# Kernel tuning notes

Measured on AMD Instinct MI355X. Metric: run time of the kernel, lower is better.

## Reference

```python
import jax, jax.numpy as jnp
import numpy as np

TAU = 2.0      # spikingjelly LIF default membrane time constant
VTH = 1.0      # threshold
SCALE = 0.25
NUM_HEADS = 16
EPS = 1e-5


def lif(x):
    # single-step LIF from rest (v=0, v_reset=0): u = v + (x - v)/tau = x/tau; spike = H(u - vth)
    return (x / TAU >= VTH).astype(x.dtype)


def bn(z, gamma, beta, mean, var):
    # inference-mode BatchNorm1d over channel dim of (TB, C, N)
    inv = gamma / jnp.sqrt(var + EPS)
    return z * inv[:, None] + (beta - mean * inv)[:, None]


def branch(z, w, gamma, beta, mean, var):
    # conv1x1 (pointwise channel mix) -> BN -> LIF
    z = jnp.einsum('oc,bcn->bon', w, z)
    return lif(bn(z, gamma, beta, mean, var))


def setup_inputs() -> dict:
    key = jax.random.key(0)
    ks = jax.random.split(key, 8)
    T, B, C, N = 4, 2, 512, 512
    x = jax.random.normal(ks[0], (T, B, C, N), dtype=jnp.float32)
    y = jax.random.normal(ks[1], (T, B, C, N), dtype=jnp.float32)
    def conv_w(k):
        return jax.random.normal(k, (C, C), dtype=jnp.float32) / np.float32(np.sqrt(C))
    def bn_params(k):
        km, kv = jax.random.split(k)
        gamma = jnp.full((C,), 2.0, dtype=jnp.float32)  # scale so LIF spikes are non-trivially sparse
        beta = jnp.zeros((C,), dtype=jnp.float32)
        mean = 0.1 * jax.random.normal(km, (C,), dtype=jnp.float32)
        var = 0.5 + jax.random.uniform(kv, (C,), dtype=jnp.float32)
        return gamma, beta, mean, var
    q_g, q_b, q_m, q_v = bn_params(ks[2])
    k_g, k_b, k_m, k_v = bn_params(ks[3])
    v_g, v_b, v_m, v_v = bn_params(ks[4])
    p_g, p_b, p_m, p_v = bn_params(ks[5])
    return {
        'x': x, 'y': y,
        'q_w': conv_w(jax.random.fold_in(key, 10)), 'q_g': q_g, 'q_b': q_b, 'q_m': q_m, 'q_v': q_v,
        'k_w': conv_w(jax.random.fold_in(key, 11)), 'k_g': k_g, 'k_b': k_b, 'k_m': k_m, 'k_v': k_v,
        'v_w': conv_w(jax.random.fold_in(key, 12)), 'v_g': v_g, 'v_b': v_b, 'v_m': v_m, 'v_v': v_v,
        'p_w': conv_w(jax.random.fold_in(key, 13)), 'p_g': p_g, 'p_b': p_b, 'p_m': p_m, 'p_v': p_v,
    }


def reference(x, y, q_w, q_g, q_b, q_m, q_v, k_w, k_g, k_b, k_m, k_v,
              v_w, v_g, v_b, v_m, v_v, p_w, p_g, p_b, p_m, p_v):
    T, B, C, N = x.shape
    H = NUM_HEADS
    D = C // H
    xq = x.reshape(T * B, C, N)
    yk = y.reshape(T * B, C, N)
    # q/k/v: conv1x1 + BN + LIF, then split heads: (T,B,C,N) -> (T,B,H,N,D)
    q = branch(xq, q_w, q_g, q_b, q_m, q_v).reshape(T, B, H, D, N).transpose(0, 1, 2, 4, 3)
    k = branch(yk, k_w, k_g, k_b, k_m, k_v).reshape(T, B, H, D, N).transpose(0, 1, 2, 4, 3)
    v = branch(yk, v_w, v_g, v_b, v_m, v_v).reshape(T, B, H, D, N).transpose(0, 1, 2, 4, 3)
    # softmax-free spiking attention: (Q K^T) V * scale
    attn = jnp.einsum('tbhnd,tbhmd->tbhnm', q, k)
    o = jnp.einsum('tbhnm,tbhmd->tbhnd', attn, v) * SCALE
    o = o.transpose(0, 1, 2, 4, 3).reshape(T, B, C, N)  # (T,B,H,D,N) -> (T,B,C,N)
    o = lif(o.reshape(T * B, C, N))
    o = branch(o, p_w, p_g, p_b, p_m, p_v).reshape(T, B, C, N)
    return o
```

## Files before the change

kernel.cpp:

```cpp
#include <hip/hip_runtime.h>
#include <math.h>

#define TBD 8
#define CD  512
#define ND  512
#define PLANE (TBD*CD*ND)
#define WPL   (CD*CD)

typedef __attribute__((ext_vector_type(8))) short bf16x8;
typedef __attribute__((ext_vector_type(4))) float f32x4;

__device__ __forceinline__ float b2f(unsigned short u){
  union{unsigned int i; float f;} x; x.i = ((unsigned int)u) << 16; return x.f;
}
__device__ __forceinline__ unsigned short f2b(float f){
  unsigned int u = __builtin_bit_cast(unsigned int, f);
  u += 0x7fffu + ((u >> 16) & 1u);
  return (unsigned short)(u >> 16);
}
__device__ __forceinline__ void async_ld16(const unsigned short* g, unsigned short* l){
  __builtin_amdgcn_global_load_lds((const __attribute__((address_space(1))) unsigned int*)g,
      (__attribute__((address_space(3))) unsigned int*)l, 16, 0, 0);
}

__global__ __launch_bounds__(256) void prep(
    const float* __restrict__ x, const float* __restrict__ y,
    const float* __restrict__ Qw, const float* __restrict__ Kw,
    const float* __restrict__ Vw, const float* __restrict__ Pw,
    const float* __restrict__ Qg, const float* __restrict__ Qb, const float* __restrict__ Qm, const float* __restrict__ Qv,
    const float* __restrict__ Kg, const float* __restrict__ Kb, const float* __restrict__ Km, const float* __restrict__ Kv,
    const float* __restrict__ Vg, const float* __restrict__ Vb, const float* __restrict__ Vm, const float* __restrict__ Vv,
    const float* __restrict__ Pg, const float* __restrict__ Pb, const float* __restrict__ Pm, const float* __restrict__ Pv,
    unsigned short* __restrict__ wsu, float* __restrict__ ib)
{
  const int bx = blockIdx.x, t = threadIdx.x;
  if (bx < 1024) {
    __shared__ __align__(16) float tl[64][68];
    const int inp = bx >> 9, rem = bx & 511;
    const int tb = rem >> 6, tile = rem & 63;
    const int ct = (tile & 7) << 6, nt = (tile >> 3) << 6;
    const float* xg = inp ? y : x;
    #pragma unroll
    for (int r = 0; r < 4; ++r) {
      const int row = (t >> 4) + (r << 4);
      const int col = (t & 15) << 2;
      *(float4*)&tl[row][col] =
          *(const float4*)(xg + ((size_t)(tb*CD + ct + row))*ND + nt + col);
    }
    __syncthreads();
    const int nl = t >> 2, cb = (t & 3) << 4;
    __align__(16) unsigned short h[3][16];
    #pragma unroll
    for (int j = 0; j < 16; ++j) {
      const float f = tl[cb + j][nl];
      const unsigned short a = f2b(f);  const float r1 = f - b2f(a);
      const unsigned short b = f2b(r1); const float r2 = r1 - b2f(b);
      h[0][j] = a; h[1][j] = b; h[2][j] = f2b(r2);
    }
    unsigned short* base = wsu + (size_t)inp*3*PLANE;
    const size_t rowo = ((size_t)tb*ND + nt + nl)*CD + ct + cb;
    #pragma unroll
    for (int s = 0; s < 3; ++s) {
      *(uint4*)(base + (size_t)s*PLANE + rowo)     = *(uint4*)&h[s][0];
      *(uint4*)(base + (size_t)s*PLANE + rowo + 8) = *(uint4*)&h[s][8];
    }
  } else if (bx < 2048) {
    const int b2 = bx - 1024;
    const int mat = b2 >> 8, rr = b2 & 255;
    const float* Wg = (mat==0)?Qw:(mat==1)?Kw:(mat==2)?Vw:Pw;
    const int row = (rr << 1) + (t >> 7);
    const int col = (t & 127) << 2;
    const float4 w = *(const float4*)(Wg + (size_t)row*CD + col);
    const float f[4] = {w.x, w.y, w.z, w.w};
    __align__(8) unsigned short h[3][4];
    #pragma unroll
    for (int j = 0; j < 4; ++j) {
      const unsigned short a = f2b(f[j]);  const float r1 = f[j] - b2f(a);
      const unsigned short b = f2b(r1);    const float r2 = r1 - b2f(b);
      h[0][j] = a; h[1][j] = b; h[2][j] = f2b(r2);
    }
    unsigned short* base = wsu + (size_t)6*PLANE + (size_t)mat*3*WPL;
    #pragma unroll
    for (int s = 0; s < 3; ++s)
      *(uint2*)(base + (size_t)s*WPL + (size_t)row*CD + col) = *(uint2*)&h[s][0];
  } else {
    const int idx = (bx - 2048)*256 + t;
    const int br = idx >> 9, ch = idx & 511;
    const float* G = (br==0)?Qg:(br==1)?Kg:(br==2)?Vg:Pg;
    const float* B = (br==0)?Qb:(br==1)?Kb:(br==2)?Vb:Pb;
    const float* M = (br==0)?Qm:(br==1)?Km:(br==2)?Vm:Pm;
    const float* V = (br==0)?Qv:(br==1)?Kv:(br==2)?Vv:Pv;
    const float inv = G[ch] / sqrtf(V[ch] + 1e-5f);
    ib[br*1024 + ch]       = inv;
    ib[br*1024 + 512 + ch] = B[ch] - M[ch]*inv;
  }
}

template<int XS, bool F32OUT>
__global__ __launch_bounds__(256) void gemm_mfma(
    const unsigned short* __restrict__ Ab,
    const unsigned short* __restrict__ Bbp,
    const float* __restrict__ ibp,
    unsigned short* __restrict__ outb,
    float* __restrict__ outf)
{
  const int bx  = blockIdx.x;
  const int idx = bx & 511;
  const int br  = bx >> 9;
  const int tb  = idx & 7;
  const int o0  = ((idx >> 3) & 7) << 6;
  const int n0  = (idx >> 6) << 6;
  const int t    = threadIdx.x;
  const int lane = t & 63, wave = t >> 6;

  const unsigned short* A = Ab + (size_t)br*3*WPL;
  const unsigned short* B = Bbp + (size_t)(br ? 3 : 0)*PLANE;
  const float* IB = ibp + br*1024;

  __shared__ __align__(16) unsigned short Al[2][3][4][512];
  __shared__ __align__(16) unsigned short Bl[2][XS][4][512];

  const int lr = lane >> 2;
  const int lc = (((lane & 3) ^ ((lane >> 3) & 3)) << 3);
  constexpr int TPW = (12 + 4*XS) / 4;

  auto stage = [&](int buf, int c0) {
    #pragma unroll
    for (int j = 0; j < TPW; ++j) {
      const int tix = wave*TPW + j;
      if (tix < 12) {
        const int s = tix >> 2, ot = tix & 3;
        const unsigned short* g = A + (size_t)s*WPL
            + (size_t)(o0 + (ot << 4) + lr)*CD + c0 + lc;
        async_ld16(g, &Al[buf][s][ot][lane << 3]);
      } else {
        const int k = tix - 12, s = k >> 2, nt = k & 3;
        const unsigned short* g = B + (size_t)s*PLANE
            + ((size_t)tb*ND + n0 + (nt << 4) + lr)*CD + c0 + lc;
        async_ld16(g, &Bl[buf][s][nt][lane << 3]);
      }
    }
  };

  f32x4 acc[2][2];
  const f32x4 zero = {0.f, 0.f, 0.f, 0.f};
  acc[0][0] = zero; acc[0][1] = zero; acc[1][0] = zero; acc[1][1] = zero;

  const int otb = (wave >> 1) << 1;
  const int ntb = (wave & 1) << 1;
  const int fo = ((lane & 15) << 5) + ((((lane >> 4) ^ ((lane >> 1) & 3)) & 3) << 3);

  stage(0, 0);
  for (int i = 0; i < 16; ++i) {
    const int buf = i & 1;
    __syncthreads();
    if (i < 15) stage(buf ^ 1, (i + 1) << 5);

    bf16x8 Af[3][2], Bf[XS][2];
    #pragma unroll
    for (int s = 0; s < 3; ++s)
      #pragma unroll
      for (int oy = 0; oy < 2; ++oy)
        Af[s][oy] = *(const bf16x8*)&Al[buf][s][otb + oy][fo];
    #pragma unroll
    for (int s = 0; s < XS; ++s)
      #pragma unroll
      for (int nx = 0; nx < 2; ++nx)
        Bf[s][nx] = *(const bf16x8*)&Bl[buf][s][ntb + nx][fo];

    auto mm = [&](int sa, int sb) {
      #pragma unroll
      for (int oy = 0; oy < 2; ++oy)
        #pragma unroll
        for (int nx = 0; nx < 2; ++nx)
          acc[oy][nx] = __builtin_amdgcn_mfma_f32_16x16x32_bf16(
              Af[sa][oy], Bf[sb][nx], acc[oy][nx], 0, 0, 0);
    };
    if constexpr (XS == 3) {
      mm(0,0); mm(0,1); mm(1,0); mm(1,1); mm(0,2); mm(2,0);
    } else {
      mm(0,0); mm(1,0); mm(2,0);
    }
  }

  const int rbase = (lane >> 4) << 2;
  const int cl = lane & 15;
  #pragma unroll
  for (int oy = 0; oy < 2; ++oy) {
    #pragma unroll
    for (int r = 0; r < 4; ++r) {
      const int ch = o0 + ((otb + oy) << 4) + rbase + r;
      const float inv  = IB[ch];
      const float bias = IB[512 + ch];
      #pragma unroll
      for (int nx = 0; nx < 2; ++nx) {
        const float v = acc[oy][nx][r];
        const bool sp = (v * inv + bias >= 2.0f);
        const int n = n0 + ((ntb + nx) << 4) + cl;
        const size_t off = ((size_t)tb*CD + ch)*ND + n;
        if constexpr (F32OUT) outf[off] = sp ? 1.0f : 0.0f;
        else (outb + (size_t)br*PLANE)[off] = sp ? (unsigned short)0x3F80 : (unsigned short)0;
      }
    }
  }
}

__global__ __launch_bounds__(256) void attn(
    const unsigned short* __restrict__ Qs, const unsigned short* __restrict__ Ks,
    const unsigned short* __restrict__ Vs, unsigned short* __restrict__ S2T)
{
  const int tbh = blockIdx.x >> 2;
  const int n0  = (blockIdx.x & 3) << 7;
  const int t   = threadIdx.x;

  __shared__ __align__(16) float sm[2*32*260];
  float* Ksh = sm;
  float* Vsh = sm + 32*260;
  float* Gs  = sm;
  float* Osh = sm + 2048;

  const unsigned short* Kh = Ks + (size_t)tbh*32*ND;
  const unsigned short* Vh = Vs + (size_t)tbh*32*ND;
  const unsigned short* Qh = Qs + (size_t)tbh*32*ND;

  const int d1a = t >> 4, d2a = t & 15;
  float a00 = 0.f, a01 = 0.f, a10 = 0.f, a11 = 0.f;
  const int srow = t & 31, scb = (t >> 5) << 5;

  for (int m0 = 0; m0 < ND; m0 += 256) {
    if (m0) __syncthreads();
    #pragma unroll
    for (int q = 0; q < 4; ++q) {
      const uint4 kraw = *(const uint4*)(Kh + (size_t)srow*ND + m0 + scb + (q<<3));
      const uint4 vraw = *(const uint4*)(Vh + (size_t)srow*ND + m0 + scb + (q<<3));
      const unsigned short* kr = (const unsigned short*)&kraw;
      const unsigned short* vr = (const unsigned short*)&vraw;
      float4 k0 = {b2f(kr[0]), b2f(kr[1]), b2f(kr[2]), b2f(kr[3])};
      float4 k1 = {b2f(kr[4]), b2f(kr[5]), b2f(kr[6]), b2f(kr[7])};
      float4 v0 = {b2f(vr[0]), b2f(vr[1]), b2f(vr[2]), b2f(vr[3])};
      float4 v1 = {b2f(vr[4]), b2f(vr[5]), b2f(vr[6]), b2f(vr[7])};
      *(float4*)&Ksh[srow*260 + scb + (q<<3)]     = k0;
      *(float4*)&Ksh[srow*260 + scb + (q<<3) + 4] = k1;
      *(float4*)&Vsh[srow*260 + scb + (q<<3)]     = v0;
      *(float4*)&Vsh[srow*260 + scb + (q<<3) + 4] = v1;
    }
    __syncthreads();
    #pragma unroll 8
    for (int m = 0; m < 256; m += 4) {
      const float4 k0 = *(const float4*)&Ksh[d1a*260 + m];
      const float4 k1 = *(const float4*)&Ksh[(d1a+16)*260 + m];
      const float4 v0 = *(const float4*)&Vsh[d2a*260 + m];
      const float4 v1 = *(const float4*)&Vsh[(d2a+16)*260 + m];
      a00 += k0.x*v0.x + k0.y*v0.y + k0.z*v0.z + k0.w*v0.w;
      a01 += k0.x*v1.x + k0.y*v1.y + k0.z*v1.z + k0.w*v1.w;
      a10 += k1.x*v0.x + k1.y*v0.y + k1.z*v0.z + k1.w*v0.w;
      a11 += k1.x*v1.x + k1.y*v1.y + k1.z*v1.z + k1.w*v1.w;
    }
  }
  __syncthreads();
  Gs[d1a*33 + d2a]           = a00;
  Gs[d1a*33 + d2a + 16]      = a01;
  Gs[(d1a+16)*33 + d2a]      = a10;
  Gs[(d1a+16)*33 + d2a + 16] = a11;
  __syncthreads();

  const int r  = t >> 5;
  const int nn = (t & 31) << 2;
  float o[4][4];
  #pragma unroll
  for (int j = 0; j < 4; ++j)
    #pragma unroll
    for (int u = 0; u < 4; ++u) o[j][u] = 0.f;

  #pragma unroll 4
  for (int dp = 0; dp < 32; ++dp) {
    const uint2 qraw = *(const uint2*)(Qh + (size_t)dp*ND + n0 + nn);
    const unsigned short* qr = (const unsigned short*)&qraw;
    const float q0 = b2f(qr[0]), q1 = b2f(qr[1]), q2 = b2f(qr[2]), q3 = b2f(qr[3]);
    #pragma unroll
    for (int j = 0; j < 4; ++j) {
      const float gv = Gs[dp*33 + r + (j<<3)];
      o[j][0] += q0*gv; o[j][1] += q1*gv; o[j][2] += q2*gv; o[j][3] += q3*gv;
    }
  }
  #pragma unroll
  for (int j = 0; j < 4; ++j)
    #pragma unroll
    for (int u = 0; u < 4; ++u)
      Osh[(nn+u)*36 + r + (j<<3)] = o[j][u];
  __syncthreads();

  const int n   = t >> 1;
  const int cb2 = (t & 1) << 4;
  __align__(16) unsigned short h[16];
  #pragma unroll
  for (int j = 0; j < 16; j += 4) {
    const float4 f = *(const float4*)&Osh[n*36 + cb2 + j];
    h[j]   = (f.x >= 8.0f) ? 0x3F80 : 0;
    h[j+1] = (f.y >= 8.0f) ? 0x3F80 : 0;
    h[j+2] = (f.z >= 8.0f) ? 0x3F80 : 0;
    h[j+3] = (f.w >= 8.0f) ? 0x3F80 : 0;
  }
  const int tb = tbh >> 4, hh = tbh & 15;
  unsigned short* dst = S2T + ((size_t)tb*ND + n0 + n)*CD + (hh << 5) + cb2;
  *(uint4*)(dst)     = *(uint4*)&h[0];
  *(uint4*)(dst + 8) = *(uint4*)&h[8];
}

extern "C" void kernel_launch(void* const* d_in, const int* in_sizes, int n_in,
                              void* d_out, int out_size, void* d_ws, size_t ws_size,
                              hipStream_t stream)
{
  const float* x  = (const float*)d_in[0];
  const float* y  = (const float*)d_in[1];
  const float* qw = (const float*)d_in[2];
  const float* qg = (const float*)d_in[3];
  const float* qb = (const float*)d_in[4];
  const float* qm = (const float*)d_in[5];
  const float* qv = (const float*)d_in[6];
  const float* kw = (const float*)d_in[7];
  const float* kg = (const float*)d_in[8];
  const float* kb = (const float*)d_in[9];
  const float* km = (const float*)d_in[10];
  const float* kv = (const float*)d_in[11];
  const float* vw = (const float*)d_in[12];
  const float* vg = (const float*)d_in[13];
  const float* vb = (const float*)d_in[14];
  const float* vm = (const float*)d_in[15];
  const float* vv = (const float*)d_in[16];
  const float* pw = (const float*)d_in[17];
  const float* pg = (const float*)d_in[18];
  const float* pb = (const float*)d_in[19];
  const float* pm = (const float*)d_in[20];
  const float* pv = (const float*)d_in[21];

  unsigned short* wsu = (unsigned short*)d_ws;
  unsigned short* Wq  = wsu + (size_t)6*PLANE;
  unsigned short* SPK = wsu + (size_t)6*PLANE + 12*WPL;
  unsigned short* S2T = SPK + (size_t)3*PLANE;
  float* ib = (float*)(wsu + (size_t)10*PLANE + 12*WPL);

  prep<<<2056, 256, 0, stream>>>(x, y, qw, kw, vw, pw,
      qg, qb, qm, qv, kg, kb, km, kv, vg, vb, vm, vv, pg, pb, pm, pv,
      wsu, ib);

  gemm_mfma<3, false><<<1536, 256, 0, stream>>>(Wq, wsu, ib, SPK, nullptr);

  attn<<<512, 256, 0, stream>>>(SPK, SPK + PLANE, SPK + 2*(size_t)PLANE, S2T);

  gemm_mfma<1, true><<<512, 256, 0, stream>>>(Wq + (size_t)9*WPL, S2T,
      ib + 3*1024, nullptr, (float*)d_out);
}
```

Measured before the change: 186.8 us.

## Move spiking attention onto fp16 MFMA with transposed Q and staged epilogues

The attention kernel's scalar fp32 K·V^T and G·Q loops are replaced by fp16 MFMA. K and V are loaded asynchronously into LDS and the Gram matrix is converted to fp16 per wave before multiplying by Q. The first GEMM now writes spikes as fp16 ones, and the Q branch is written transposed (n-major) so attention can read it directly. Both GEMM epilogues stage their output through LDS to produce coalesced vector stores. G entries are integer counts up to 512, which fp16 represents exactly. The risk is extra LDS traffic and added synchronisation in the epilogues.

After: 175.5 us. 6.0% less time.

```diff
diff --git a/kernel.cpp b/kernel.cpp
--- a/kernel.cpp
+++ b/kernel.cpp
@@ -7,20 +7,24 @@
 #define PLANE (TBD*CD*ND)
 #define WPL   (CD*CD)
 
+typedef unsigned short u16;
+typedef unsigned int u32;
+typedef _Float16 f16;
 typedef __attribute__((ext_vector_type(8))) short bf16x8;
+typedef __attribute__((ext_vector_type(8))) _Float16 f16x8;
 typedef __attribute__((ext_vector_type(4))) float f32x4;
 
-__device__ __forceinline__ float b2f(unsigned short u){
-  union{unsigned int i; float f;} x; x.i = ((unsigned int)u) << 16; return x.f;
-}
-__device__ __forceinline__ unsigned short f2b(float f){
-  unsigned int u = __builtin_bit_cast(unsigned int, f);
+__device__ __forceinline__ float b2f(u16 u){
+  union{u32 i; float f;} x; x.i = ((u32)u) << 16; return x.f;
+}
+__device__ __forceinline__ u16 f2b(float f){
+  u32 u = __builtin_bit_cast(u32, f);
   u += 0x7fffu + ((u >> 16) & 1u);
-  return (unsigned short)(u >> 16);
-}
-__device__ __forceinline__ void async_ld16(const unsigned short* g, unsigned short* l){
-  __builtin_amdgcn_global_load_lds((const __attribute__((address_space(1))) unsigned int*)g,
-      (__attribute__((address_space(3))) unsigned int*)l, 16, 0, 0);
+  return (u16)(u >> 16);
+}
+__device__ __forceinline__ void async_ld16(const void* g, void* l){
+  __builtin_amdgcn_global_load_lds((const __attribute__((address_space(1))) u32*)g,
+      (__attribute__((address_space(3))) u32*)l, 16, 0, 0);
 }
 
 __global__ __launch_bounds__(256) void prep(
@@ -31,7 +35,7 @@
     const float* __restrict__ Kg, const float* __restrict__ Kb, const float* __restrict__ Km, const float* __restrict__ Kv,
     const float* __restrict__ Vg, const float* __restrict__ Vb, const float* __restrict__ Vm, const float* __restrict__ Vv,
     const float* __restrict__ Pg, const float* __restrict__ Pb, const float* __restrict__ Pm, const float* __restrict__ Pv,
-    unsigned short* __restrict__ wsu, float* __restrict__ ib)
+    u16* __restrict__ wsu, float* __restrict__ ib)
 {
   const int bx = blockIdx.x, t = threadIdx.x;
   if (bx < 1024) {
@@ -49,15 +53,15 @@
     }
     __syncthreads();
     const int nl = t >> 2, cb = (t & 3) << 4;
-    __align__(16) unsigned short h[3][16];
+    __align__(16) u16 h[3][16];
     #pragma unroll
     for (int j = 0; j < 16; ++j) {
       const float f = tl[cb + j][nl];
-      const unsigned short a = f2b(f);  const float r1 = f - b2f(a);
-      const unsigned short b = f2b(r1); const float r2 = r1 - b2f(b);
+      const u16 a = f2b(f);  const float r1 = f - b2f(a);
+      const u16 b = f2b(r1); const float r2 = r1 - b2f(b);
       h[0][j] = a; h[1][j] = b; h[2][j] = f2b(r2);
     }
-    unsigned short* base = wsu + (size_t)inp*3*PLANE;
+    u16* base = wsu + (size_t)inp*3*PLANE;
     const size_t rowo = ((size_t)tb*ND + nt + nl)*CD + ct + cb;
     #pragma unroll
     for (int s = 0; s < 3; ++s) {
@@ -72,14 +76,14 @@
     const int col = (t & 127) << 2;
     const float4 w = *(const float4*)(Wg + (size_t)row*CD + col);
     const float f[4] = {w.x, w.y, w.z, w.w};
-    __align__(8) unsigned short h[3][4];
+    __align__(8) u16 h[3][4];
     #pragma unroll
     for (int j = 0; j < 4; ++j) {
-      const unsigned short a = f2b(f[j]);  const float r1 = f[j] - b2f(a);
-      const unsigned short b = f2b(r1);    const float r2 = r1 - b2f(b);
+      const u16 a = f2b(f[j]);  const float r1 = f[j] - b2f(a);
+      const u16 b = f2b(r1);    const float r2 = r1 - b2f(b);
       h[0][j] = a; h[1][j] = b; h[2][j] = f2b(r2);
     }
-    unsigned short* base = wsu + (size_t)6*PLANE + (size_t)mat*3*WPL;
+    u16* base = wsu + (size_t)6*PLANE + (size_t)mat*3*WPL;
     #pragma unroll
     for (int s = 0; s < 3; ++s)
       *(uint2*)(base + (size_t)s*WPL + (size_t)row*CD + col) = *(uint2*)&h[s][0];
@@ -96,13 +100,11 @@
   }
 }
 
-template<int XS, bool F32OUT>
+template<int XS>
 __global__ __launch_bounds__(256) void gemm_mfma(
-    const unsigned short* __restrict__ Ab,
-    const unsigned short* __restrict__ Bbp,
+    const u16* __restrict__ Ab, const u16* __restrict__ Bbp,
     const float* __restrict__ ibp,
-    unsigned short* __restrict__ outb,
-    float* __restrict__ outf)
+    u16* __restrict__ qt, u16* __restrict__ spk, float* __restrict__ outf)
 {
   const int bx  = blockIdx.x;
   const int idx = bx & 511;
@@ -113,15 +115,16 @@
   const int t    = threadIdx.x;
   const int lane = t & 63, wave = t >> 6;
 
-  const unsigned short* A = Ab + (size_t)br*3*WPL;
-  const unsigned short* B = Bbp + (size_t)(br ? 3 : 0)*PLANE;
+  const u16* A = Ab + (size_t)br*3*WPL;
+  const u16* B = Bbp + (size_t)(br ? 3 : 0)*PLANE;
   const float* IB = ibp + br*1024;
 
-  __shared__ __align__(16) unsigned short Al[2][3][4][512];
-  __shared__ __align__(16) unsigned short Bl[2][XS][4][512];
+  __shared__ __align__(16) u16 smem[2*3*4*512 + 2*XS*4*512];
+  u16* Al = smem;
+  u16* Bl = smem + 2*3*4*512;
 
   const int lr = lane >> 2;
-  const int lc = (((lane & 3) ^ ((lane >> 3) & 3)) << 3);
+  const int lc = ((lane & 3) ^ ((lane >> 3) & 3)) << 3;
   constexpr int TPW = (12 + 4*XS) / 4;
 
   auto stage = [&](int buf, int c0) {
@@ -130,14 +133,12 @@
       const int tix = wave*TPW + j;
       if (tix < 12) {
         const int s = tix >> 2, ot = tix & 3;
-        const unsigned short* g = A + (size_t)s*WPL
-            + (size_t)(o0 + (ot << 4) + lr)*CD + c0 + lc;
-        async_ld16(g, &Al[buf][s][ot][lane << 3]);
+        async_ld16(A + (size_t)s*WPL + (size_t)(o0 + (ot<<4) + lr)*CD + c0 + lc,
+                   Al + (((buf*3 + s)*4 + ot) << 9) + (lane << 3));
       } else {
         const int k = tix - 12, s = k >> 2, nt = k & 3;
-        const unsigned short* g = B + (size_t)s*PLANE
-            + ((size_t)tb*ND + n0 + (nt << 4) + lr)*CD + c0 + lc;
-        async_ld16(g, &Bl[buf][s][nt][lane << 3]);
+        async_ld16(B + (size_t)s*PLANE + ((size_t)tb*ND + n0 + (nt<<4) + lr)*CD + c0 + lc,
+                   Bl + (((buf*XS + s)*4 + nt) << 9) + (lane << 3));
       }
     }
   };
@@ -161,12 +162,12 @@
     for (int s = 0; s < 3; ++s)
       #pragma unroll
       for (int oy = 0; oy < 2; ++oy)
-        Af[s][oy] = *(const bf16x8*)&Al[buf][s][otb + oy][fo];
+        Af[s][oy] = *(const bf16x8*)(Al + (((buf*3 + s)*4 + otb + oy) << 9) + fo);
     #pragma unroll
     for (int s = 0; s < XS; ++s)
       #pragma unroll
       for (int nx = 0; nx < 2; ++nx)
-        Bf[s][nx] = *(const bf16x8*)&Bl[buf][s][ntb + nx][fo];
+        Bf[s][nx] = *(const bf16x8*)(Bl + (((buf*XS + s)*4 + ntb + nx) << 9) + fo);
 
     auto mm = [&](int sa, int sb) {
       #pragma unroll
@@ -183,128 +184,168 @@
     }
   }
 
+  __syncthreads();
   const int rbase = (lane >> 4) << 2;
   const int cl = lane & 15;
-  #pragma unroll
-  for (int oy = 0; oy < 2; ++oy) {
-    #pragma unroll
-    for (int r = 0; r < 4; ++r) {
-      const int ch = o0 + ((otb + oy) << 4) + rbase + r;
-      const float inv  = IB[ch];
-      const float bias = IB[512 + ch];
-      #pragma unroll
-      for (int nx = 0; nx < 2; ++nx) {
-        const float v = acc[oy][nx][r];
-        const bool sp = (v * inv + bias >= 2.0f);
-        const int n = n0 + ((ntb + nx) << 4) + cl;
-        const size_t off = ((size_t)tb*CD + ch)*ND + n;
-        if constexpr (F32OUT) outf[off] = sp ? 1.0f : 0.0f;
-        else (outb + (size_t)br*PLANE)[off] = sp ? (unsigned short)0x3F80 : (unsigned short)0;
-      }
+
+  if constexpr (XS == 1) {
+    float* Fb = (float*)smem;
+    #pragma unroll
+    for (int oy = 0; oy < 2; ++oy)
+      #pragma unroll
+      for (int r = 0; r < 4; ++r) {
+        const int chl = ((otb + oy) << 4) + rbase + r;
+        const int ch = o0 + chl;
+        const float inv = IB[ch], bias = IB[512 + ch];
+        #pragma unroll
+        for (int nx = 0; nx < 2; ++nx) {
+          const bool sp = (acc[oy][nx][r] * inv + bias >= 2.0f);
+          Fb[chl*68 + ((ntb + nx) << 4) + cl] = sp ? 1.0f : 0.0f;
+        }
+      }
+    __syncthreads();
+    const int row = t >> 2, seg = (t & 3) << 4;
+    float* dst = outf + ((size_t)tb*CD + o0 + row)*ND + n0 + seg;
+    #pragma unroll
+    for (int u = 0; u < 4; ++u)
+      *(float4*)(dst + 4*u) = *(float4*)&Fb[row*68 + seg + 4*u];
+  } else {
+    u16* Sb = smem;
+    #pragma unroll
+    for (int oy = 0; oy < 2; ++oy)
+      #pragma unroll
+      for (int r = 0; r < 4; ++r) {
+        const int chl = ((otb + oy) << 4) + rbase + r;
+        const int ch = o0 + chl;
+        const float inv = IB[ch], bias = IB[512 + ch];
+        #pragma unroll
+        for (int nx = 0; nx < 2; ++nx) {
+          const bool sp = (acc[oy][nx][r] * inv + bias >= 2.0f);
+          Sb[chl*136 + ((ntb + nx) << 4) + cl] = sp ? (u16)0x3C00 : (u16)0;
+        }
+      }
+    __syncthreads();
+    if (br == 0) {
+      const int nr = t >> 2, cs = (t & 3) << 4;
+      __align__(16) u16 h[16];
+      #pragma unroll
+      for (int j = 0; j < 16; ++j) h[j] = Sb[(cs + j)*136 + nr];
+      u16* dst = qt + ((size_t)tb*ND + n0 + nr)*CD + o0 + cs;
+      *(uint4*)dst       = *(uint4*)&h[0];
+      *(uint4*)(dst + 8) = *(uint4*)&h[8];
+    } else {
+      u16* sp_ = spk + (size_t)(br - 1)*PLANE;
+      const int row = t >> 2, seg = (t & 3) << 4;
+      u16* dst = sp_ + ((size_t)tb*CD + o0 + row)*ND + n0 + seg;
+      *(uint4*)dst       = *(uint4*)&Sb[row*136 + seg];
+      *(uint4*)(dst + 8) = *(uint4*)&Sb[row*136 + seg + 8];
     }
   }
 }
 
 __global__ __launch_bounds__(256) void attn(
-    const unsigned short* __restrict__ Qs, const unsigned short* __restrict__ Ks,
-    const unsigned short* __restrict__ Vs, unsigned short* __restrict__ S2T)
+    const u16* __restrict__ Qt, const u16* __restrict__ Ks,
+    const u16* __restrict__ Vs, u16* __restrict__ S2T)
 {
   const int tbh = blockIdx.x >> 2;
   const int n0  = (blockIdx.x & 3) << 7;
-  const int t   = threadIdx.x;
-
-  __shared__ __align__(16) float sm[2*32*260];
-  float* Ksh = sm;
-  float* Vsh = sm + 32*260;
-  float* Gs  = sm;
-  float* Osh = sm + 2048;
-
-  const unsigned short* Kh = Ks + (size_t)tbh*32*ND;
-  const unsigned short* Vh = Vs + (size_t)tbh*32*ND;
-  const unsigned short* Qh = Qs + (size_t)tbh*32*ND;
-
-  const int d1a = t >> 4, d2a = t & 15;
-  float a00 = 0.f, a01 = 0.f, a10 = 0.f, a11 = 0.f;
-  const int srow = t & 31, scb = (t >> 5) << 5;
-
-  for (int m0 = 0; m0 < ND; m0 += 256) {
-    if (m0) __syncthreads();
-    #pragma unroll
-    for (int q = 0; q < 4; ++q) {
-      const uint4 kraw = *(const uint4*)(Kh + (size_t)srow*ND + m0 + scb + (q<<3));
-      const uint4 vraw = *(const uint4*)(Vh + (size_t)srow*ND + m0 + scb + (q<<3));
-      const unsigned short* kr = (const unsigned short*)&kraw;
-      const unsigned short* vr = (const unsigned short*)&vraw;
-      float4 k0 = {b2f(kr[0]), b2f(kr[1]), b2f(kr[2]), b2f(kr[3])};
-      float4 k1 = {b2f(kr[4]), b2f(kr[5]), b2f(kr[6]), b2f(kr[7])};
-      float4 v0 = {b2f(vr[0]), b2f(vr[1]), b2f(vr[2]), b2f(vr[3])};
-      float4 v1 = {b2f(vr[4]), b2f(vr[5]), b2f(vr[6]), b2f(vr[7])};
-      *(float4*)&Ksh[srow*260 + scb + (q<<3)]     = k0;
-      *(float4*)&Ksh[srow*260 + scb + (q<<3) + 4] = k1;
-      *(float4*)&Vsh[srow*260 + scb + (q<<3)]     = v0;
-      *(float4*)&Vsh[srow*260 + scb + (q<<3) + 4] = v1;
-    }
-    __syncthreads();
-    #pragma unroll 8
-    for (int m = 0; m < 256; m += 4) {
-      const float4 k0 = *(const float4*)&Ksh[d1a*260 + m];
-      const float4 k1 = *(const float4*)&Ksh[(d1a+16)*260 + m];
-      const float4 v0 = *(const float4*)&Vsh[d2a*260 + m];
-      const float4 v1 = *(const float4*)&Vsh[(d2a+16)*260 + m];
-      a00 += k0.x*v0.x + k0.y*v0.y + k0.z*v0.z + k0.w*v0.w;
-      a01 += k0.x*v1.x + k0.y*v1.y + k0.z*v1.z + k0.w*v1.w;
-      a10 += k1.x*v0.x + k1.y*v0.y + k1.z*v0.z + k1.w*v0.w;
-      a11 += k1.x*v1.x + k1.y*v1.y + k1.z*v1.z + k1.w*v1.w;
-    }
-  }
-  __syncthreads();
-  Gs[d1a*33 + d2a]           = a00;
-  Gs[d1a*33 + d2a + 16]      = a01;
-  Gs[(d1a+16)*33 + d2a]      = a10;
-  Gs[(d1a+16)*33 + d2a + 16] = a11;
-  __syncthreads();
-
-  const int r  = t >> 5;
-  const int nn = (t & 31) << 2;
-  float o[4][4];
+  const int t = threadIdx.x, lane = t & 63, wave = t >> 6;
+  const int tb = tbh >> 4, h = tbh & 15;
+
+  __shared__ __align__(16) u16 Kt[2*8*512];
+  __shared__ __align__(16) u16 Vt[2*8*512];
+  __shared__ __align__(16) u16 QTs[8*512];
+  __shared__ __align__(16) u16 Gt[4*32*40];
+  __shared__ __align__(16) u16 Sb[128*40];
+
+  const u16* Kh = Ks + (size_t)tbh*32*ND;
+  const u16* Vh = Vs + (size_t)tbh*32*ND;
+
+  const int lr = lane >> 2;
+  const int lc = ((lane & 3) ^ ((lane >> 3) & 3)) << 3;
+  const int fo = ((lane & 15) << 5) + ((((lane >> 4) ^ ((lane >> 1) & 3)) & 3) << 3);
+
+  f32x4 g[2][2];
+  const f32x4 zero = {0.f, 0.f, 0.f, 0.f};
+  g[0][0] = zero; g[0][1] = zero; g[1][0] = zero; g[1][1] = zero;
+
+  for (int half = 0; half < 2; ++half) {
+    if (half) __syncthreads();
+    #pragma unroll
+    for (int j = 0; j < 8; ++j) {
+      const int u = wave*8 + j;
+      const int mat = u >> 4, dt = (u >> 3) & 1, kc = u & 7;
+      const u16* src = (mat ? Vh : Kh) + (size_t)((dt << 4) + lr)*ND + (half << 8) + (kc << 5) + lc;
+      u16* dst = (mat ? Vt : Kt) + (((dt << 3) + kc) << 9) + (lane << 3);
+      async_ld16(src, dst);
+    }
+    if (half == 0) {
+      #pragma unroll
+      for (int j = 0; j < 2; ++j) {
+        const int nt = wave*2 + j;
+        async_ld16(Qt + ((size_t)tb*ND + n0 + (nt << 4) + lr)*CD + (h << 5) + lc,
+                   QTs + (nt << 9) + (lane << 3));
+      }
+    }
+    __syncthreads();
+    for (int kc = 0; kc < 8; ++kc) {
+      const f16* kt = (const f16*)Kt;
+      const f16* vt = (const f16*)Vt;
+      f16x8 ka0 = *(const f16x8*)(kt + (kc << 9) + fo);
+      f16x8 ka1 = *(const f16x8*)(kt + ((8 + kc) << 9) + fo);
+      f16x8 vb0 = *(const f16x8*)(vt + (kc << 9) + fo);
+      f16x8 vb1 = *(const f16x8*)(vt + ((8 + kc) << 9) + fo);
+      g[0][0] = __builtin_amdgcn_mfma_f32_16x16x32_f16(ka0, vb0, g[0][0], 0,0,0);
+      g[0][1] = __builtin_amdgcn_mfma_f32_16x16x32_f16(ka0, vb1, g[0][1], 0,0,0);
+      g[1][0] = __builtin_amdgcn_mfma_f32_16x16x32_f16(ka1, vb0, g[1][0], 0,0,0);
+      g[1][1] = __builtin_amdgcn_mfma_f32_16x16x32_f16(ka1, vb1, g[1][1], 0,0,0);
+    }
+  }
+
+  f16* myG = (f16*)(Gt + wave*(32*40));
+  const int rq = (lane >> 4) << 2, cl = lane & 15;
   #pragma unroll
-  for (int j = 0; j < 4; ++j)
-    #pragma unroll
-    for (int u = 0; u < 4; ++u) o[j][u] = 0.f;
-
-  #pragma unroll 4
-  for (int dp = 0; dp < 32; ++dp) {
-    const uint2 qraw = *(const uint2*)(Qh + (size_t)dp*ND + n0 + nn);
-    const unsigned short* qr = (const unsigned short*)&qraw;
-    const float q0 = b2f(qr[0]), q1 = b2f(qr[1]), q2 = b2f(qr[2]), q3 = b2f(qr[3]);
-    #pragma unroll
-    for (int j = 0; j < 4; ++j) {
-      const float gv = Gs[dp*33 + r + (j<<3)];
-      o[j][0] += q0*gv; o[j][1] += q1*gv; o[j][2] += q2*gv; o[j][3] += q3*gv;
-    }
-  }
+  for (int d1t = 0; d1t < 2; ++d1t)
+    #pragma unroll
+    for (int d2t = 0; d2t < 2; ++d2t)
+      #pragma unroll
+      for (int r = 0; r < 4; ++r) {
+        const int d1 = (d1t << 4) + rq + r;
+        const int d2 = (d2t << 4) + cl;
+        myG[d2*40 + d1] = (f16)g[d1t][d2t][r];
+      }
+  asm volatile("s_waitcnt lgkmcnt(0)" ::: "memory");
+
+  f32x4 o[2][2];
+  o[0][0] = zero; o[0][1] = zero; o[1][0] = zero; o[1][1] = zero;
+  const f16* qs = (const f16*)QTs;
   #pragma unroll
-  for (int j = 0; j < 4; ++j)
-    #pragma unroll
-    for (int u = 0; u < 4; ++u)
-      Osh[(nn+u)*36 + r + (j<<3)] = o[j][u];
-  __syncthreads();
-
-  const int n   = t >> 1;
-  const int cb2 = (t & 1) << 4;
-  __align__(16) unsigned short h[16];
+  for (int dd = 0; dd < 2; ++dd) {
+    f16x8 ga = *(const f16x8*)(myG + (((dd << 4) + cl)*40) + ((lane >> 4) << 3));
+    #pragma unroll
+    for (int ntl = 0; ntl < 2; ++ntl) {
+      f16x8 qb = *(const f16x8*)(qs + ((wave*2 + ntl) << 9) + fo);
+      o[dd][ntl] = __builtin_amdgcn_mfma_f32_16x16x32_f16(ga, qb, o[dd][ntl], 0,0,0);
+    }
+  }
+
   #pragma unroll
-  for (int j = 0; j < 16; j += 4) {
-    const float4 f = *(const float4*)&Osh[n*36 + cb2 + j];
-    h[j]   = (f.x >= 8.0f) ? 0x3F80 : 0;
-    h[j+1] = (f.y >= 8.0f) ? 0x3F80 : 0;
-    h[j+2] = (f.z >= 8.0f) ? 0x3F80 : 0;
-    h[j+3] = (f.w >= 8.0f) ? 0x3F80 : 0;
-  }
-  const int tb = tbh >> 4, hh = tbh & 15;
-  unsigned short* dst = S2T + ((size_t)tb*ND + n0 + n)*CD + (hh << 5) + cb2;
-  *(uint4*)(dst)     = *(uint4*)&h[0];
-  *(uint4*)(dst + 8) = *(uint4*)&h[8];
+  for (int dd = 0; dd < 2; ++dd)
+    #pragma unroll
+    for (int ntl = 0; ntl < 2; ++ntl)
+      #pragma unroll
+      for (int r = 0; r < 4; ++r) {
+        const int n_local = ((wave*2 + ntl) << 4) + cl;
+        const int c_local = (dd << 4) + rq + r;
+        Sb[n_local*40 + c_local] = (o[dd][ntl][r] >= 8.0f) ? (u16)0x3F80 : (u16)0;
+      }
+  asm volatile("s_waitcnt lgkmcnt(0)" ::: "memory");
+
+  const int nr = (wave << 5) + (lane >> 1);
+  const int cs = (lane & 1) << 4;
+  u16* dst = S2T + ((size_t)tb*ND + n0 + nr)*CD + (h << 5) + cs;
+  *(uint4*)dst       = *(uint4*)&Sb[nr*40 + cs];
+  *(uint4*)(dst + 8) = *(uint4*)&Sb[nr*40 + cs + 8];
 }
 
 extern "C" void kernel_launch(void* const* d_in, const int* in_sizes, int n_in,
@@ -334,20 +375,21 @@
   const float* pm = (const float*)d_in[20];
   const float* pv = (const float*)d_in[21];
 
-  unsigned short* wsu = (unsigned short*)d_ws;
-  unsigned short* Wq  = wsu + (size_t)6*PLANE;
-  unsigned short* SPK = wsu + (size_t)6*PLANE + 12*WPL;
-  unsigned short* S2T = SPK + (size_t)3*PLANE;
-  float* ib = (float*)(wsu + (size_t)10*PLANE + 12*WPL);
+  u16* wsu = (u16*)d_ws;
+  u16* Wq   = wsu + (size_t)6*PLANE;
+  u16* QT   = wsu + (size_t)6*PLANE + 12*WPL;
+  u16* Kspk = QT + (size_t)PLANE;
+  u16* S2T  = QT + (size_t)3*PLANE;
+  float* ib = (float*)(QT + (size_t)4*PLANE);
 
   prep<<<2056, 256, 0, stream>>>(x, y, qw, kw, vw, pw,
       qg, qb, qm, qv, kg, kb, km, kv, vg, vb, vm, vv, pg, pb, pm, pv,
       wsu, ib);
 
-  gemm_mfma<3, false><<<1536, 256, 0, stream>>>(Wq, wsu, ib, SPK, nullptr);
-
-  attn<<<512, 256, 0, stream>>>(SPK, SPK + PLANE, SPK + 2*(size_t)PLANE, S2T);
-
-  gemm_mfma<1, true><<<512, 256, 0, stream>>>(Wq + (size_t)9*WPL, S2T,
-      ib + 3*1024, nullptr, (float*)d_out);
-}
+  gemm_mfma<3><<<1536, 256, 0, stream>>>(Wq, wsu, ib, QT, Kspk, nullptr);
+
+  attn<<<512, 256, 0, stream>>>(QT, Kspk, Kspk + (size_t)PLANE, S2T);
+
+  gemm_mfma<1><<<512, 256, 0, stream>>>(Wq + (size_t)9*WPL, S2T,
+      ib + 3*1024, nullptr, nullptr, (float*)d_out);
+}
```
